# Kernel optimization log

Measured on AMD Instinct MI355X. Metric: run time of the kernel, lower is better.

## Reference

```python
import jax, jax.numpy as jnp
import numpy as np

N = 50000
E = 500000
D = 512


def setup_inputs() -> dict:
    key = jax.random.key(0)
    ks = jax.random.split(key, 16)
    inp = {
        'h': jax.random.normal(ks[0], (N, D), jnp.float32),
        's': jax.random.normal(ks[1], (N, D), jnp.float32),
        'm': jax.random.normal(ks[2], (N, D), jnp.float32),
        'norm_g': jax.random.uniform(ks[3], (N, 1), jnp.float32),
        'norm_f': jax.random.uniform(ks[4], (N, 1), jnp.float32),
        'src_g': jax.random.randint(ks[5], (E,), 0, N, jnp.int32),
        'dst_g': jax.random.randint(ks[6], (E,), 0, N, jnp.int32),
        'src_f': jax.random.randint(ks[7], (E,), 0, N, jnp.int32),
        'dst_f': jax.random.randint(ks[8], (E,), 0, N, jnp.int32),
        'wh': jax.random.normal(ks[9], (D, D), jnp.float32) / np.sqrt(D),
        'ws': jax.random.normal(ks[10], (D, D), jnp.float32) / np.sqrt(D),
        'wm': jax.random.normal(ks[11], (D, D), jnp.float32) / np.sqrt(D),
        'bh': jax.random.normal(ks[12], (D,), jnp.float32) * 0.02,
        'bs': jax.random.normal(ks[13], (D,), jnp.float32) * 0.02,
        'bm': jax.random.normal(ks[14], (D,), jnp.float32) * 0.02,
    }
    return inp


def reference(h, s, m, norm_g, norm_f, src_g, dst_g, src_f, dst_f, wh, ws, wm, bh, bs, bm):
    n = h.shape[0]
    # dense projections
    h = (h @ wh) * norm_g          # [N,D]
    s = (s @ ws) * norm_f          # [N,D]
    m = m @ wm                     # [N,D] global skip
    # dual GCN aggregation: copy_src + sum over edges, then norm scaling
    h = jax.ops.segment_sum(h[src_g], dst_g, num_segments=n) * norm_g
    s = jax.ops.segment_sum(s[src_f], dst_f, num_segments=n) * norm_f
    # bias add + three-way residual sum + activation
    out = (h + bh) + (s + bs) + (m + bm)
    return jax.nn.relu(out)
```

## Files before the change

### kernel.cpp

```cpp
#include <hip/hip_runtime.h>
#include <hip/hip_bf16.h>
#include <cstdint>
#include <cstddef>

#define DD 512
#define D4 128

typedef unsigned short u16;
typedef unsigned int u32;
typedef short s8v __attribute__((ext_vector_type(8)));
typedef float f4v __attribute__((ext_vector_type(4)));

__device__ __forceinline__ u16 f2bf(float f) {
  u32 u = __builtin_bit_cast(u32, f);
  u = (u + 0x7FFFu + ((u >> 16) & 1u)) >> 16;
  return (u16)u;
}
__device__ __forceinline__ float bf2f(u16 h) {
  u32 u = ((u32)h) << 16;
  return __builtin_bit_cast(float, u);
}

__device__ __forceinline__ void glds16(const void* g, void* l) {
  __builtin_amdgcn_global_load_lds(
      (const __attribute__((address_space(1))) void*)g,
      (__attribute__((address_space(3))) void*)l, 16, 0, 0);
}


__global__ void hist_kernel(const int* __restrict__ dg, const int* __restrict__ df,
                            int* __restrict__ deg_g, int* __restrict__ deg_f, int E) {
  int i = blockIdx.x * blockDim.x + threadIdx.x;
  int total = 2 * E;
  int stride = gridDim.x * blockDim.x;
  for (; i < total; i += stride) {
    if (i < E) atomicAdd(&deg_g[dg[i]], 1);
    else       atomicAdd(&deg_f[df[i - E]], 1);
  }
}

__global__ void scan_kernel(const int* __restrict__ deg_g, const int* __restrict__ deg_f,
                            int* __restrict__ rp_g, int* __restrict__ rp_f,
                            int* __restrict__ cur_g, int* __restrict__ cur_f, int N) {
  const int* deg = (blockIdx.x == 0) ? deg_g : deg_f;
  int* rp  = (blockIdx.x == 0) ? rp_g  : rp_f;
  int* cur = (blockIdx.x == 0) ? cur_g : cur_f;
  __shared__ int sums[256];
  int t = threadIdx.x;
  int strip = (N + 255) / 256;
  int base = t * strip;
  int lim = N - base; if (lim > strip) lim = strip; if (lim < 0) lim = 0;
  int s = 0;
  for (int j = 0; j < lim; ++j) s += deg[base + j];
  sums[t] = s;
  __syncthreads();
  for (int off = 1; off < 256; off <<= 1) {
    int v = sums[t];
    int add = (t >= off) ? sums[t - off] : 0;
    __syncthreads();
    sums[t] = v + add;
    __syncthreads();
  }
  int run = (t == 0) ? 0 : sums[t - 1];
  for (int j = 0; j < lim; ++j) {
    rp[base + j] = run;
    cur[base + j] = run;
    run += deg[base + j];
  }
  if (t == 255) rp[N] = sums[255];
}

__global__ void fill_kernel(const int* __restrict__ src, const int* __restrict__ dst,
                            int* __restrict__ cur, int* __restrict__ csr, int E) {
  int i = blockIdx.x * blockDim.x + threadIdx.x;
  int stride = gridDim.x * blockDim.x;
  for (; i < E; i += stride) {
    int d = dst[i];
    int pos = atomicAdd(&cur[d], 1);
    csr[pos] = src[i];
  }
}


__global__ __launch_bounds__(128) void gather_kernel(const float* __restrict__ feat,
    const float* __restrict__ norm, const int* __restrict__ rp, const int* __restrict__ csr,
    u16* __restrict__ XHi, u16* __restrict__ XLo, int N) {
  int i = blockIdx.x;
  if (i >= N) return;
  int c = threadIdx.x;
  const float4* f4 = (const float4*)feat;
  float4 acc = make_float4(0.f, 0.f, 0.f, 0.f);
  int b = rp[i], e = rp[i + 1];
  int j = b;
  for (; j + 4 <= e; j += 4) {
    int s0 = csr[j], s1 = csr[j + 1], s2 = csr[j + 2], s3 = csr[j + 3];
    float g0 = norm[s0], g1 = norm[s1], g2 = norm[s2], g3 = norm[s3];
    float4 v0 = f4[(size_t)s0 * D4 + c];
    float4 v1 = f4[(size_t)s1 * D4 + c];
    float4 v2 = f4[(size_t)s2 * D4 + c];
    float4 v3 = f4[(size_t)s3 * D4 + c];
    acc.x += g0 * v0.x + g1 * v1.x + g2 * v2.x + g3 * v3.x;
    acc.y += g0 * v0.y + g1 * v1.y + g2 * v2.y + g3 * v3.y;
    acc.z += g0 * v0.z + g1 * v1.z + g2 * v2.z + g3 * v3.z;
    acc.w += g0 * v0.w + g1 * v1.w + g2 * v2.w + g3 * v3.w;
  }
  for (; j < e; ++j) {
    int s = csr[j];
    float gs = norm[s];
    float4 v = f4[(size_t)s * D4 + c];
    acc.x += gs * v.x; acc.y += gs * v.y; acc.z += gs * v.z; acc.w += gs * v.w;
  }
  float gi = norm[i];
  float o0 = acc.x * gi, o1 = acc.y * gi, o2 = acc.z * gi, o3 = acc.w * gi;
  u16 h0 = f2bf(o0), h1 = f2bf(o1), h2 = f2bf(o2), h3 = f2bf(o3);
  ushort4 hv = make_ushort4(h0, h1, h2, h3);
  ushort4 lv = make_ushort4(f2bf(o0 - bf2f(h0)), f2bf(o1 - bf2f(h1)),
                            f2bf(o2 - bf2f(h2)), f2bf(o3 - bf2f(h3)));
  *(ushort4*)(XHi + (size_t)i * DD + c * 4) = hv;
  *(ushort4*)(XLo + (size_t)i * DD + c * 4) = lv;
}


__global__ __launch_bounds__(256) void wsplit_kernel(
    const float* __restrict__ wh, const float* __restrict__ ws, const float* __restrict__ wm,
    u16* __restrict__ WtHi, u16* __restrict__ WtLo) {
  __shared__ float tile[64][65];
  int si = blockIdx.y;
  const float* W = (si == 0) ? wh : (si == 1) ? ws : wm;
  int tb = blockIdx.x;
  int kb = (tb >> 3) << 6;
  int cb = (tb & 7) << 6;
  int t = threadIdx.x;
#pragma unroll
  for (int i = 0; i < 16; ++i) {
    int idx = t + (i << 8);
    int kr = idx >> 6, cc = idx & 63;
    tile[kr][cc] = W[(size_t)(kb + kr) * DD + cb + cc];
  }
  __syncthreads();
  size_t base = (size_t)si * DD * DD;
#pragma unroll
  for (int i = 0; i < 16; ++i) {
    int idx = t + (i << 8);
    int cr = idx >> 6, kk = idx & 63;
    float v = tile[kk][cr];
    u16 hi = f2bf(v);
    u16 lo = f2bf(v - bf2f(hi));
    size_t off = base + (size_t)(cb + cr) * DD + kb + kk;
    WtHi[off] = hi;
    WtLo[off] = lo;
  }
}


#define BM 128
#define BN 256
#define BK 32

__global__ __launch_bounds__(256, 2) void gemm3_mfma(
    const u16* __restrict__ XhHi, const u16* __restrict__ XhLo,
    const u16* __restrict__ XsHi, const u16* __restrict__ XsLo,
    const float* __restrict__ Mm,
    const u16* __restrict__ WtHi, const u16* __restrict__ WtLo,
    const float* __restrict__ bh, const float* __restrict__ bs, const float* __restrict__ bm,
    float* __restrict__ out, int Mrows) {
  __shared__ u16 sAh[BM * BK];
  __shared__ u16 sAl[BM * BK];
  __shared__ u16 sBh[BN * BK];
  __shared__ u16 sBl[BN * BK];

  int tid = threadIdx.x;
  int wv = tid >> 6;
  int lane = tid & 63;
  int bm0 = blockIdx.y * BM;
  int bn0 = blockIdx.x * BN;

  f4v acc[8][4];
#pragma unroll
  for (int i = 0; i < 8; ++i)
#pragma unroll
    for (int j = 0; j < 4; ++j) acc[i][j] = (f4v){0.f, 0.f, 0.f, 0.f};

  for (int si = 0; si < 3; ++si) {
    const u16* AH = (si == 0) ? XhHi : XsHi;
    const u16* AL = (si == 0) ? XhLo : XsLo;
    const u16* WH = WtHi + (size_t)si * DD * DD;
    const u16* WL = WtLo + (size_t)si * DD * DD;
    for (int k0 = 0; k0 < DD; k0 += BK) {
      {
        int colo = lane >> 2;
        int chunk = lane & 3;
#pragma unroll
        for (int i = 0; i < 4; ++i) {
          int cg = wv * 4 + i;
          int col = cg * 16 + colo;
          const u16* gh = WH + (size_t)(bn0 + col) * DD + k0 + chunk * 8;
          const u16* gl = WL + (size_t)(bn0 + col) * DD + k0 + chunk * 8;
          glds16(gh, (char*)sBh + cg * 1024);
          glds16(gl, (char*)sBl + cg * 1024);
        }
      }
      if (si < 2) {
        int rowo = lane >> 2;
        int chunk = lane & 3;
#pragma unroll
        for (int i = 0; i < 2; ++i) {
          int rg = wv * 2 + i;
          int row = rg * 16 + rowo;
          const u16* gh = AH + (size_t)(bm0 + row) * DD + k0 + chunk * 8;
          const u16* gl = AL + (size_t)(bm0 + row) * DD + k0 + chunk * 8;
          glds16(gh, (char*)sAh + rg * 1024);
          glds16(gl, (char*)sAl + rg * 1024);
        }
      } else {
        float4 vv[4];
#pragma unroll
        for (int i = 0; i < 4; ++i) {
          int idx = tid + (i << 8);
          int row = idx >> 3;
          int gr = bm0 + row;
          int kc = idx & 7;
          vv[i] = make_float4(0.f, 0.f, 0.f, 0.f);
          if (gr < Mrows) vv[i] = *(const float4*)(Mm + (size_t)gr * DD + k0 + kc * 4);
        }
#pragma unroll
        for (int i = 0; i < 4; ++i) {
          int idx = tid + (i << 8);
          int row = idx >> 3;
          int kc = idx & 7;
          float4 v = vv[i];
          u16 h0 = f2bf(v.x), h1 = f2bf(v.y), h2 = f2bf(v.z), h3 = f2bf(v.w);
          u16 l0 = f2bf(v.x - bf2f(h0)), l1 = f2bf(v.y - bf2f(h1));
          u16 l2 = f2bf(v.z - bf2f(h2)), l3 = f2bf(v.w - bf2f(h3));
          uint2 ph = make_uint2((u32)h0 | ((u32)h1 << 16), (u32)h2 | ((u32)h3 << 16));
          uint2 pl = make_uint2((u32)l0 | ((u32)l1 << 16), (u32)l2 | ((u32)l3 << 16));
          *(uint2*)(sAh + row * BK + kc * 4) = ph;
          *(uint2*)(sAl + row * BK + kc * 4) = pl;
        }
      }
      __syncthreads();
      int kchunk = (lane >> 4) * 8;
      int rr = lane & 15;
      s8v bhf[4], blf[4];
#pragma unroll
      for (int ng = 0; ng < 4; ++ng) {
        int col = wv * 64 + ng * 16 + rr;
        bhf[ng] = *(const s8v*)(sBh + col * BK + kchunk);
        blf[ng] = *(const s8v*)(sBl + col * BK + kchunk);
      }
#pragma unroll
      for (int mg = 0; mg < 8; ++mg) {
        int row = mg * 16 + rr;
        s8v ah = *(const s8v*)(sAh + row * BK + kchunk);
        s8v al = *(const s8v*)(sAl + row * BK + kchunk);
#pragma unroll
        for (int ng = 0; ng < 4; ++ng) {
          acc[mg][ng] = __builtin_amdgcn_mfma_f32_16x16x32_bf16(ah, bhf[ng], acc[mg][ng], 0, 0, 0);
          acc[mg][ng] = __builtin_amdgcn_mfma_f32_16x16x32_bf16(al, bhf[ng], acc[mg][ng], 0, 0, 0);
          acc[mg][ng] = __builtin_amdgcn_mfma_f32_16x16x32_bf16(ah, blf[ng], acc[mg][ng], 0, 0, 0);
        }
      }
      __syncthreads();
    }
  }

  int rr = lane & 15;
  int rgrp = lane >> 4;
  float bias[4];
#pragma unroll
  for (int ng = 0; ng < 4; ++ng) {
    int col = bn0 + wv * 64 + ng * 16 + rr;
    bias[ng] = bh[col] + bs[col] + bm[col];
  }
#pragma unroll
  for (int mg = 0; mg < 8; ++mg) {
#pragma unroll
    for (int r = 0; r < 4; ++r) {
      int row = bm0 + mg * 16 + rgrp * 4 + r;
      if (row < Mrows) {
#pragma unroll
        for (int ng = 0; ng < 4; ++ng) {
          int col = bn0 + wv * 64 + ng * 16 + rr;
          float v = acc[mg][ng][r] + bias[ng];
          out[(size_t)row * DD + col] = v > 0.f ? v : 0.f;
        }
      }
    }
  }
}


extern "C" void kernel_launch(void* const* d_in, const int* in_sizes, int n_in,
                              void* d_out, int out_size, void* d_ws, size_t ws_size,
                              hipStream_t stream) {
  const float* h   = (const float*)d_in[0];
  const float* s   = (const float*)d_in[1];
  const float* m   = (const float*)d_in[2];
  const float* ng  = (const float*)d_in[3];
  const float* nf  = (const float*)d_in[4];
  const int* src_g = (const int*)d_in[5];
  const int* dst_g = (const int*)d_in[6];
  const int* src_f = (const int*)d_in[7];
  const int* dst_f = (const int*)d_in[8];
  const float* wh  = (const float*)d_in[9];
  const float* wsp = (const float*)d_in[10];
  const float* wm  = (const float*)d_in[11];
  const float* bh  = (const float*)d_in[12];
  const float* bs  = (const float*)d_in[13];
  const float* bm  = (const float*)d_in[14];
  float* out = (float*)d_out;

  int N = in_sizes[3];
  int E = in_sizes[5];
  int Npad = (N + BM - 1) & ~(BM - 1);

  u16* XhHi = (u16*)d_ws;
  u16* XhLo = XhHi + (size_t)Npad * DD;
  u16* XsHi = XhLo + (size_t)Npad * DD;
  u16* XsLo = XsHi + (size_t)Npad * DD;
  u16* WtHi = XsLo + (size_t)Npad * DD;
  u16* WtLo = WtHi + (size_t)3 * DD * DD;
  int* deg_g = (int*)(WtLo + (size_t)3 * DD * DD);
  int* deg_f = deg_g + N;
  int* rp_g  = deg_f + N;
  int* rp_f  = rp_g + (N + 1);
  int* cur_g = rp_f + (N + 1);
  int* cur_f = cur_g + N;
  int* csr_g = cur_f + N;
  int* csr_f = csr_g + E;

  hipMemsetAsync(deg_g, 0, 2 * (size_t)N * sizeof(int), stream);
  wsplit_kernel<<<dim3(64, 3), 256, 0, stream>>>(wh, wsp, wm, WtHi, WtLo);
  hist_kernel<<<2048, 256, 0, stream>>>(dst_g, dst_f, deg_g, deg_f, E);
  scan_kernel<<<2, 256, 0, stream>>>(deg_g, deg_f, rp_g, rp_f, cur_g, cur_f, N);
  fill_kernel<<<2048, 256, 0, stream>>>(src_g, dst_g, cur_g, csr_g, E);
  fill_kernel<<<2048, 256, 0, stream>>>(src_f, dst_f, cur_f, csr_f, E);
  gather_kernel<<<N, 128, 0, stream>>>(h, ng, rp_g, csr_g, XhHi, XhLo, N);
  gather_kernel<<<N, 128, 0, stream>>>(s, nf, rp_f, csr_f, XsHi, XsLo, N);

  dim3 gg(DD / BN, (N + BM - 1) / BM);
  gemm3_mfma<<<gg, 256, 0, stream>>>(XhHi, XhLo, XsHi, XsLo, m, WtHi, WtLo,
                                     bh, bs, bm, out, N);
}
```

Before: 1.095 ms.

## Gather from bf16 copies of features and XOR-swizzle GEMM LDS tiles

Raw h and s features are first converted to a bf16 buffer, and the edge gather then reads 8-byte rows instead of 16-byte ones, halving random gather traffic. This adds a full read/write conversion pass per feature matrix and drops the input's low mantissa bits, a precision loss versus the previous hi/lo split. Separately, the GEMM's LDS A/B tiles use an XOR swizzle on 16-byte chunks to reduce bank conflicts. The A-row loads are clamped to the last valid row so the unpadded workspace can be used.

```diff
diff --git a/kernel.cpp b/kernel.cpp
--- a/kernel.cpp
+++ b/kernel.cpp
@@ -82,36 +82,48 @@
 }
 
 
-__global__ __launch_bounds__(128) void gather_kernel(const float* __restrict__ feat,
+__global__ __launch_bounds__(256) void conv_bf16_kernel(const float* __restrict__ in,
+                                                        u16* __restrict__ outb, int total4) {
+  int i = blockIdx.x * blockDim.x + threadIdx.x;
+  int stride = gridDim.x * blockDim.x;
+  for (; i < total4; i += stride) {
+    float4 v = ((const float4*)in)[i];
+    ushort4 o = make_ushort4(f2bf(v.x), f2bf(v.y), f2bf(v.z), f2bf(v.w));
+    ((ushort4*)outb)[i] = o;
+  }
+}
+
+
+__global__ __launch_bounds__(128) void gather_kernel(const u16* __restrict__ featb,
     const float* __restrict__ norm, const int* __restrict__ rp, const int* __restrict__ csr,
     u16* __restrict__ XHi, u16* __restrict__ XLo, int N) {
   int i = blockIdx.x;
   if (i >= N) return;
   int c = threadIdx.x;
-  const float4* f4 = (const float4*)feat;
-  float4 acc = make_float4(0.f, 0.f, 0.f, 0.f);
+  const ushort4* f8 = (const ushort4*)featb;
+  float a0 = 0.f, a1 = 0.f, a2 = 0.f, a3 = 0.f;
   int b = rp[i], e = rp[i + 1];
   int j = b;
   for (; j + 4 <= e; j += 4) {
     int s0 = csr[j], s1 = csr[j + 1], s2 = csr[j + 2], s3 = csr[j + 3];
     float g0 = norm[s0], g1 = norm[s1], g2 = norm[s2], g3 = norm[s3];
-    float4 v0 = f4[(size_t)s0 * D4 + c];
-    float4 v1 = f4[(size_t)s1 * D4 + c];
-    float4 v2 = f4[(size_t)s2 * D4 + c];
-    float4 v3 = f4[(size_t)s3 * D4 + c];
-    acc.x += g0 * v0.x + g1 * v1.x + g2 * v2.x + g3 * v3.x;
-    acc.y += g0 * v0.y + g1 * v1.y + g2 * v2.y + g3 * v3.y;
-    acc.z += g0 * v0.z + g1 * v1.z + g2 * v2.z + g3 * v3.z;
-    acc.w += g0 * v0.w + g1 * v1.w + g2 * v2.w + g3 * v3.w;
+    ushort4 v0 = f8[(size_t)s0 * D4 + c];
+    ushort4 v1 = f8[(size_t)s1 * D4 + c];
+    ushort4 v2 = f8[(size_t)s2 * D4 + c];
+    ushort4 v3 = f8[(size_t)s3 * D4 + c];
+    a0 += g0 * bf2f(v0.x) + g1 * bf2f(v1.x) + g2 * bf2f(v2.x) + g3 * bf2f(v3.x);
+    a1 += g0 * bf2f(v0.y) + g1 * bf2f(v1.y) + g2 * bf2f(v2.y) + g3 * bf2f(v3.y);
+    a2 += g0 * bf2f(v0.z) + g1 * bf2f(v1.z) + g2 * bf2f(v2.z) + g3 * bf2f(v3.z);
+    a3 += g0 * bf2f(v0.w) + g1 * bf2f(v1.w) + g2 * bf2f(v2.w) + g3 * bf2f(v3.w);
   }
   for (; j < e; ++j) {
     int s = csr[j];
     float gs = norm[s];
-    float4 v = f4[(size_t)s * D4 + c];
-    acc.x += gs * v.x; acc.y += gs * v.y; acc.z += gs * v.z; acc.w += gs * v.w;
+    ushort4 v = f8[(size_t)s * D4 + c];
+    a0 += gs * bf2f(v.x); a1 += gs * bf2f(v.y); a2 += gs * bf2f(v.z); a3 += gs * bf2f(v.w);
   }
   float gi = norm[i];
-  float o0 = acc.x * gi, o1 = acc.y * gi, o2 = acc.z * gi, o3 = acc.w * gi;
+  float o0 = a0 * gi, o1 = a1 * gi, o2 = a2 * gi, o3 = a3 * gi;
   u16 h0 = f2bf(o0), h1 = f2bf(o1), h2 = f2bf(o2), h3 = f2bf(o3);
   ushort4 hv = make_ushort4(h0, h1, h2, h3);
   ushort4 lv = make_ushort4(f2bf(o0 - bf2f(h0)), f2bf(o1 - bf2f(h1)),
@@ -193,9 +205,10 @@
 #pragma unroll
         for (int i = 0; i < 4; ++i) {
           int cg = wv * 4 + i;
-          int col = cg * 16 + colo;
-          const u16* gh = WH + (size_t)(bn0 + col) * DD + k0 + chunk * 8;
-          const u16* gl = WL + (size_t)(bn0 + col) * DD + k0 + chunk * 8;
+          int lcol = cg * 16 + colo;
+          int sw = (lcol >> 1) & 3;
+          const u16* gh = WH + (size_t)(bn0 + lcol) * DD + k0 + ((chunk ^ sw) * 8);
+          const u16* gl = WL + (size_t)(bn0 + lcol) * DD + k0 + ((chunk ^ sw) * 8);
           glds16(gh, (char*)sBh + cg * 1024);
           glds16(gl, (char*)sBl + cg * 1024);
         }
@@ -206,9 +219,12 @@
 #pragma unroll
         for (int i = 0; i < 2; ++i) {
           int rg = wv * 2 + i;
-          int row = rg * 16 + rowo;
-          const u16* gh = AH + (size_t)(bm0 + row) * DD + k0 + chunk * 8;
-          const u16* gl = AL + (size_t)(bm0 + row) * DD + k0 + chunk * 8;
+          int lrow = rg * 16 + rowo;
+          int sw = (lrow >> 1) & 3;
+          int grow = bm0 + lrow;
+          if (grow >= Mrows) grow = Mrows - 1;
+          const u16* gh = AH + (size_t)grow * DD + k0 + ((chunk ^ sw) * 8);
+          const u16* gl = AL + (size_t)grow * DD + k0 + ((chunk ^ sw) * 8);
           glds16(gh, (char*)sAh + rg * 1024);
           glds16(gl, (char*)sAl + rg * 1024);
         }
@@ -228,31 +244,35 @@
           int idx = tid + (i << 8);
           int row = idx >> 3;
           int kc = idx & 7;
+          int sw = (row >> 1) & 3;
+          int off = row * 32 + (((kc >> 1) ^ sw) * 8) + (kc & 1) * 4;
           float4 v = vv[i];
           u16 h0 = f2bf(v.x), h1 = f2bf(v.y), h2 = f2bf(v.z), h3 = f2bf(v.w);
           u16 l0 = f2bf(v.x - bf2f(h0)), l1 = f2bf(v.y - bf2f(h1));
           u16 l2 = f2bf(v.z - bf2f(h2)), l3 = f2bf(v.w - bf2f(h3));
           uint2 ph = make_uint2((u32)h0 | ((u32)h1 << 16), (u32)h2 | ((u32)h3 << 16));
           uint2 pl = make_uint2((u32)l0 | ((u32)l1 << 16), (u32)l2 | ((u32)l3 << 16));
-          *(uint2*)(sAh + row * BK + kc * 4) = ph;
-          *(uint2*)(sAl + row * BK + kc * 4) = pl;
+          *(uint2*)(sAh + off) = ph;
+          *(uint2*)(sAl + off) = pl;
         }
       }
       __syncthreads();
-      int kchunk = (lane >> 4) * 8;
+      int c16 = lane >> 4;
       int rr = lane & 15;
       s8v bhf[4], blf[4];
 #pragma unroll
       for (int ng = 0; ng < 4; ++ng) {
         int col = wv * 64 + ng * 16 + rr;
-        bhf[ng] = *(const s8v*)(sBh + col * BK + kchunk);
-        blf[ng] = *(const s8v*)(sBl + col * BK + kchunk);
+        int sw = (col >> 1) & 3;
+        bhf[ng] = *(const s8v*)(sBh + col * 32 + ((c16 ^ sw) * 8));
+        blf[ng] = *(const s8v*)(sBl + col * 32 + ((c16 ^ sw) * 8));
       }
 #pragma unroll
       for (int mg = 0; mg < 8; ++mg) {
         int row = mg * 16 + rr;
-        s8v ah = *(const s8v*)(sAh + row * BK + kchunk);
-        s8v al = *(const s8v*)(sAl + row * BK + kchunk);
+        int sw = (row >> 1) & 3;
+        s8v ah = *(const s8v*)(sAh + row * 32 + ((c16 ^ sw) * 8));
+        s8v al = *(const s8v*)(sAl + row * 32 + ((c16 ^ sw) * 8));
 #pragma unroll
         for (int ng = 0; ng < 4; ++ng) {
           acc[mg][ng] = __builtin_amdgcn_mfma_f32_16x16x32_bf16(ah, bhf[ng], acc[mg][ng], 0, 0, 0);
@@ -312,13 +332,13 @@
 
   int N = in_sizes[3];
   int E = in_sizes[5];
-  int Npad = (N + BM - 1) & ~(BM - 1);
 
   u16* XhHi = (u16*)d_ws;
-  u16* XhLo = XhHi + (size_t)Npad * DD;
-  u16* XsHi = XhLo + (size_t)Npad * DD;
-  u16* XsLo = XsHi + (size_t)Npad * DD;
-  u16* WtHi = XsLo + (size_t)Npad * DD;
+  u16* XhLo = XhHi + (size_t)N * DD;
+  u16* XsHi = XhLo + (size_t)N * DD;
+  u16* XsLo = XsHi + (size_t)N * DD;
+  u16* featb = XsLo + (size_t)N * DD;
+  u16* WtHi = featb + (size_t)N * DD;
   u16* WtLo = WtHi + (size_t)3 * DD * DD;
   int* deg_g = (int*)(WtLo + (size_t)3 * DD * DD);
   int* deg_f = deg_g + N;
@@ -329,14 +349,18 @@
   int* csr_g = cur_f + N;
   int* csr_f = csr_g + E;
 
+  int total4 = (N * DD) / 4;
+
   hipMemsetAsync(deg_g, 0, 2 * (size_t)N * sizeof(int), stream);
   wsplit_kernel<<<dim3(64, 3), 256, 0, stream>>>(wh, wsp, wm, WtHi, WtLo);
   hist_kernel<<<2048, 256, 0, stream>>>(dst_g, dst_f, deg_g, deg_f, E);
   scan_kernel<<<2, 256, 0, stream>>>(deg_g, deg_f, rp_g, rp_f, cur_g, cur_f, N);
   fill_kernel<<<2048, 256, 0, stream>>>(src_g, dst_g, cur_g, csr_g, E);
   fill_kernel<<<2048, 256, 0, stream>>>(src_f, dst_f, cur_f, csr_f, E);
-  gather_kernel<<<N, 128, 0, stream>>>(h, ng, rp_g, csr_g, XhHi, XhLo, N);
-  gather_kernel<<<N, 128, 0, stream>>>(s, nf, rp_f, csr_f, XsHi, XsLo, N);
+  conv_bf16_kernel<<<2048, 256, 0, stream>>>(h, featb, total4);
+  gather_kernel<<<N, 128, 0, stream>>>(featb, ng, rp_g, csr_g, XhHi, XhLo, N);
+  conv_bf16_kernel<<<2048, 256, 0, stream>>>(s, featb, total4);
+  gather_kernel<<<N, 128, 0, stream>>>(featb, nf, rp_f, csr_f, XsHi, XsLo, N);
 
   dim3 gg(DD / BN, (N + BM - 1) / BM);
   gemm3_mfma<<<gg, 256, 0, stream>>>(XhHi, XhLo, XsHi, XsLo, m, WtHi, WtLo,
```

Measured after the change: 985.3 us. 1.11x faster.
